# Kernel optimization log

Hardware: AMD Instinct MI355X
Metric: run time of the kernel (lower is better)

Reference implementation:

```python
import jax, jax.numpy as jnp
import numpy as np
from jax import lax

B, T = 2048, 256
V, E, H = 128, 128, 64
POS_WEIGHT = 20.0


def setup_inputs() -> dict:
    key = jax.random.key(0)
    ks = jax.random.split(key, 9)
    # indices in [1, V) so padding_idx=0 row (zeroed) is unused
    x = jax.random.randint(ks[0], (B, T), 1, V)
    targets = (jax.random.uniform(ks[1], (B,)) < 0.05).astype(jnp.float32)
    emb = jax.random.normal(ks[2], (V, E), dtype=jnp.float32).at[0].set(0.0)  # padding_idx=0
    k = 1.0 / np.sqrt(H)
    W_ih = jax.random.uniform(ks[3], (4 * H, E), minval=-k, maxval=k, dtype=jnp.float32)
    W_hh = jax.random.uniform(ks[4], (4 * H, H), minval=-k, maxval=k, dtype=jnp.float32)
    b_ih = jax.random.uniform(ks[5], (4 * H,), minval=-k, maxval=k, dtype=jnp.float32)
    b_hh = jax.random.uniform(ks[6], (4 * H,), minval=-k, maxval=k, dtype=jnp.float32)
    W_fc = jax.random.uniform(ks[7], (1, H), minval=-k, maxval=k, dtype=jnp.float32)
    b_fc = jax.random.uniform(ks[8], (1,), minval=-k, maxval=k, dtype=jnp.float32)
    return {"x": x, "targets": targets, "emb": emb, "W_ih": W_ih, "W_hh": W_hh,
            "b_ih": b_ih, "b_hh": b_hh, "W_fc": W_fc, "b_fc": b_fc}


def reference(x, targets, emb, W_ih, W_hh, b_ih, b_hh, W_fc, b_fc):
    xe = emb[x]  # [B, T, E]
    # precompute input-to-hidden projections for all timesteps: [B, T, 4H]
    xp = jnp.einsum('bte,ge->btg', xe, W_ih) + b_ih + b_hh
    h0 = jnp.zeros((xe.shape[0], W_hh.shape[1]), dtype=xe.dtype)
    c0 = jnp.zeros_like(h0)

    def step(carry, xt):
        h, c = carry
        gates = xt + h @ W_hh.T  # [B, 4H], PyTorch gate order: i, f, g, o
        i, f, g, o = jnp.split(gates, 4, axis=-1)
        c = jax.nn.sigmoid(f) * c + jax.nn.sigmoid(i) * jnp.tanh(g)
        h = jax.nn.sigmoid(o) * jnp.tanh(c)
        return (h, c), None

    (hT, _), _ = lax.scan(step, (h0, c0), jnp.swapaxes(xp, 0, 1))  # scan over time
    logits = (hT @ W_fc.T + b_fc)[:, 0]  # [B]
    # BCEWithLogits with pos_weight, mean reduction (numerically stable)
    loss = -(POS_WEIGHT * targets * jax.nn.log_sigmoid(logits)
             + (1.0 - targets) * jax.nn.log_sigmoid(-logits)).mean()
    return logits, loss
```

## Files before the change

### kernel.cpp

```cpp
#include <hip/hip_runtime.h>
#include <stdint.h>

#define B_ 2048
#define T_ 256
#define V_ 128
#define E_ 128
#define H_ 64
#define G4_ 256
#define POS_W 20.0f
#define MB_ 4
#define NBLK_ (B_ / MB_)
typedef _Float16 half1;
typedef __attribute__((ext_vector_type(8))) _Float16 f16x8;
typedef __attribute__((ext_vector_type(4))) float f32x4;

#if __has_builtin(__builtin_amdgcn_exp2f)
#define EXP2F(x) __builtin_amdgcn_exp2f(x)
#else
#define EXP2F(x) exp2f(x)
#endif

#if __has_builtin(__builtin_amdgcn_rcpf)
#define RCPF(x) __builtin_amdgcn_rcpf(x)
#else
#define RCPF(x) (1.0f / (x))
#endif

__device__ __forceinline__ float sigm(float x) {
    return RCPF(1.0f + EXP2F(-1.44269504f * x));
}
__device__ __forceinline__ float tanhr(float x) {
    float t = EXP2F(2.88539008f * x);
    return 1.0f - 2.0f * RCPF(t + 1.0f);
}

__device__ __forceinline__ void lds_barrier() {
    asm volatile("s_waitcnt lgkmcnt(0)\n\ts_barrier" ::: "memory");
}

__global__ void k_prep(const float* __restrict__ emb, const float* __restrict__ Wih,
                       const float* __restrict__ bih, const float* __restrict__ bhh,
                       float* __restrict__ projC, float* __restrict__ loss_slot) {
    int tid = threadIdx.x;
    int v = blockIdx.x;
    if (v == 0 && tid == 0) *loss_slot = 0.0f;
    int u = tid >> 2, g = tid & 3;
    int row = g * 64 + u;
    const float4* e4 = (const float4*)(emb + v * E_);
    const float4* w4 = (const float4*)(Wih + row * E_);
    float acc = bih[row] + bhh[row];
#pragma unroll
    for (int i = 0; i < E_ / 4; ++i) {
        float4 a = e4[i];
        float4 b = w4[i];
        acc += a.x * b.x + a.y * b.y + a.z * b.z + a.w * b.w;
    }
    projC[v * G4_ + tid] = acc;
}

__launch_bounds__(256, 2)
__global__ void k_lstm(const int* __restrict__ x, const float* __restrict__ Whh,
                       const float* __restrict__ projC, const float* __restrict__ Wfc,
                       const float* __restrict__ bfc, const float* __restrict__ targets,
                       float* __restrict__ logits, float* __restrict__ loss_slot) {
    int b0 = blockIdx.x * MB_;
    int t = threadIdx.x;
    int w = t >> 6, l = t & 63;
    int q = l >> 4, cc = l & 15;
    int u = 16 * w + cc;

    __shared__ __align__(16) half1 hf[2][1024];
    __shared__ int xT[T_][MB_];
    __shared__ float hfin[MB_][68];
    __shared__ float zred[MB_];

#pragma unroll
    for (int i = 0; i < MB_; ++i) xT[t][i] = x[(b0 + i) * T_ + t] << 10;
    ((float*)hf)[t] = 0.0f;
    ((float*)hf)[t + 256] = 0.0f;
    ((float*)hf)[t + 512] = 0.0f;
    ((float*)hf)[t + 768] = 0.0f;
    __syncthreads();

    f16x8 bf[4][2];
#pragma unroll
    for (int jj = 0; jj < 4; ++jj) {
#pragma unroll
        for (int c = 0; c < 2; ++c) {
            int row = jj * 64 + 16 * w + cc;
            int kb = c * 32 + q * 8;
            float4 w0 = *(const float4*)(Whh + row * H_ + kb);
            float4 w1 = *(const float4*)(Whh + row * H_ + kb + 4);
            f16x8 tmp;
            tmp[0] = (half1)w0.x; tmp[1] = (half1)w0.y;
            tmp[2] = (half1)w0.z; tmp[3] = (half1)w0.w;
            tmp[4] = (half1)w1.x; tmp[5] = (half1)w1.y;
            tmp[6] = (half1)w1.z; tmp[7] = (half1)w1.w;
            bf[jj][c] = tmp;
        }
    }

    int hbase = (u >> 5) * 512 + ((u >> 3) & 3) * 128 + (4 * q) * 8 + (u & 7);

    float cA = 0.0f, hA = 0.0f;
    const char* pcb = (const char*)projC;
    int uoff = u << 4;

    f32x4 ppA = *(const f32x4*)(pcb + xT[0][q] + uoff);
    f32x4 pnA = *(const f32x4*)(pcb + xT[1][q] + uoff);
    int xcA = xT[2][q];

    const f32x4 z4 = {0.0f, 0.0f, 0.0f, 0.0f};
    int p = 0;
#pragma unroll 2
    for (int step = 0; step < T_; ++step) {
        const f16x8 a0 = *(const f16x8*)(hf[p] + l * 8);
        const f16x8 a1 = *(const f16x8*)(hf[p] + 512 + l * 8);

        float gA[4];
#pragma unroll
        for (int jj = 0; jj < 4; ++jj) {
            f32x4 c4 = z4;
            c4[0] = ppA[jj];
            f32x4 d0 = __builtin_amdgcn_mfma_f32_16x16x32_f16(a0, bf[jj][0], c4, 0, 0, 0);
            f32x4 d1 = __builtin_amdgcn_mfma_f32_16x16x32_f16(a1, bf[jj][1], z4, 0, 0, 0);
            gA[jj] = d0[0] + d1[0];
        }

        f32x4 p2A = *(const f32x4*)(pcb + xcA + uoff);
        int xnA = xT[(step + 3) & (T_ - 1)][q];

        float iA = sigm(gA[0]);
        float fA = sigm(gA[1]);
        float ggA = tanhr(gA[2]);
        float oA = sigm(gA[3]);
        cA = fA * cA + iA * ggA;
        hA = oA * tanhr(cA);

        hf[p ^ 1][hbase] = (half1)hA;

        ppA = pnA;
        pnA = p2A;
        xcA = xnA;
        p ^= 1;
        lds_barrier();
    }

    hfin[q][u] = hA;
    __syncthreads();
    int m4 = t >> 6, uu = t & 63;
    float part = hfin[m4][uu] * Wfc[uu];
#pragma unroll
    for (int off = 32; off > 0; off >>= 1) part += __shfl_down(part, off, 64);
    if (uu == 0) {
        float z = part + bfc[0];
        logits[b0 + m4] = z;
        float tg = targets[b0 + m4];
        float e = EXP2F(-1.44269504f * fabsf(z));
        float lsp = fminf(z, 0.0f) - log1pf(e);
        float lsn = lsp - z;
        zred[m4] = -(POS_W * tg * lsp + (1.0f - tg) * lsn) * (1.0f / (float)B_);
    }
    __syncthreads();
    if (t == 0) {
        float s = 0.0f;
#pragma unroll
        for (int i = 0; i < MB_; ++i) s += zred[i];
        atomicAdd(loss_slot, s);
    }
}

extern "C" void kernel_launch(void* const* d_in, const int* in_sizes, int n_in,
                              void* d_out, int out_size, void* d_ws, size_t ws_size,
                              hipStream_t stream) {
    const int* x = (const int*)d_in[0];
    const float* targets = (const float*)d_in[1];
    const float* emb = (const float*)d_in[2];
    const float* Wih = (const float*)d_in[3];
    const float* Whh = (const float*)d_in[4];
    const float* bih = (const float*)d_in[5];
    const float* bhh = (const float*)d_in[6];
    const float* Wfc = (const float*)d_in[7];
    const float* bfc = (const float*)d_in[8];
    float* out = (float*)d_out;

    float* projC = (float*)d_ws;

    k_prep<<<dim3(V_), dim3(256), 0, stream>>>(emb, Wih, bih, bhh, projC, out + B_);
    k_lstm<<<dim3(NBLK_), dim3(256), 0, stream>>>(x, Whh, projC, Wfc, bfc, targets, out,
                                                  out + B_);
}
```

Baseline: 158.2 us.

## Ping-pong two batch groups per block to overlap MFMA with cell math

Each block now handles 8 sequences with 512 threads, split into two groups of 4 waves that run out of phase: while one group issues the recurrent MFMAs, the other computes gate nonlinearities and the cell update. Each group keeps its own h buffer, and the input projection is folded into the exponent argument instead of the MFMA accumulator. The goal is to hide MFMA latency behind transcendental ALU work inside the serial time loop. The cost is two barriers per step instead of one and half as many blocks, with occupancy now capped at one 512-thread block per CU by the launch bounds.

```diff
diff --git a/kernel.cpp b/kernel.cpp
--- a/kernel.cpp
+++ b/kernel.cpp
@@ -8,7 +8,7 @@
 #define H_ 64
 #define G4_ 256
 #define POS_W 20.0f
-#define MB_ 4
+#define MB_ 8
 #define NBLK_ (B_ / MB_)
 typedef _Float16 half1;
 typedef __attribute__((ext_vector_type(8))) _Float16 f16x8;
@@ -26,13 +26,7 @@
 #define RCPF(x) (1.0f / (x))
 #endif
 
-__device__ __forceinline__ float sigm(float x) {
-    return RCPF(1.0f + EXP2F(-1.44269504f * x));
-}
-__device__ __forceinline__ float tanhr(float x) {
-    float t = EXP2F(2.88539008f * x);
-    return 1.0f - 2.0f * RCPF(t + 1.0f);
-}
+#define L2E 1.44269504f
 
 __device__ __forceinline__ void lds_barrier() {
     asm volatile("s_waitcnt lgkmcnt(0)\n\ts_barrier" ::: "memory");
@@ -58,7 +52,7 @@
     projC[v * G4_ + tid] = acc;
 }
 
-__launch_bounds__(256, 2)
+__launch_bounds__(512, 1)
 __global__ void k_lstm(const int* __restrict__ x, const float* __restrict__ Whh,
                        const float* __restrict__ projC, const float* __restrict__ Wfc,
                        const float* __restrict__ bfc, const float* __restrict__ targets,
@@ -66,20 +60,22 @@
     int b0 = blockIdx.x * MB_;
     int t = threadIdx.x;
     int w = t >> 6, l = t & 63;
+    int g = w >> 2, wg = w & 3;
     int q = l >> 4, cc = l & 15;
-    int u = 16 * w + cc;
+    int u = 16 * wg + cc;
+    int r = g * 4 + q;
 
     __shared__ __align__(16) half1 hf[2][1024];
     __shared__ int xT[T_][MB_];
     __shared__ float hfin[MB_][68];
     __shared__ float zred[MB_];
 
-#pragma unroll
-    for (int i = 0; i < MB_; ++i) xT[t][i] = x[(b0 + i) * T_ + t] << 10;
+    for (int i = t; i < T_ * MB_; i += 512) {
+        int tt = i >> 3, rr = i & 7;
+        xT[tt][rr] = x[(b0 + rr) * T_ + tt] << 10;
+    }
     ((float*)hf)[t] = 0.0f;
-    ((float*)hf)[t + 256] = 0.0f;
     ((float*)hf)[t + 512] = 0.0f;
-    ((float*)hf)[t + 768] = 0.0f;
     __syncthreads();
 
     f16x8 bf[4][2];
@@ -87,7 +83,7 @@
     for (int jj = 0; jj < 4; ++jj) {
 #pragma unroll
         for (int c = 0; c < 2; ++c) {
-            int row = jj * 64 + 16 * w + cc;
+            int row = jj * 64 + 16 * wg + cc;
             int kb = c * 32 + q * 8;
             float4 w0 = *(const float4*)(Whh + row * H_ + kb);
             float4 w1 = *(const float4*)(Whh + row * H_ + kb + 4);
@@ -102,64 +98,84 @@
 
     int hbase = (u >> 5) * 512 + ((u >> 3) & 3) * 128 + (4 * q) * 8 + (u & 7);
 
-    float cA = 0.0f, hA = 0.0f;
+    float creg = 0.0f, hreg = 0.0f;
     const char* pcb = (const char*)projC;
     int uoff = u << 4;
 
-    f32x4 ppA = *(const f32x4*)(pcb + xT[0][q] + uoff);
-    f32x4 pnA = *(const f32x4*)(pcb + xT[1][q] + uoff);
-    int xcA = xT[2][q];
-
+    f32x4 pp = *(const f32x4*)(pcb + xT[0][r] + uoff);
+    f32x4 pn = *(const f32x4*)(pcb + xT[1][r] + uoff);
+    int xc = xT[2][r];
+
+    f32x4 d0[4], d1[4];
+    float psx = 0.f, psy = 0.f, pgz = 0.f, psw = 0.f;
     const f32x4 z4 = {0.0f, 0.0f, 0.0f, 0.0f};
-    int p = 0;
-#pragma unroll 2
+
+#define MFMA_HALF(STEP_)                                                              \
+    do {                                                                              \
+        const f16x8 a0 = *(const f16x8*)(hf[g] + l * 8);                              \
+        const f16x8 a1 = *(const f16x8*)(hf[g] + 512 + l * 8);                        \
+        _Pragma("unroll") for (int jj = 0; jj < 4; ++jj) {                            \
+            d0[jj] = __builtin_amdgcn_mfma_f32_16x16x32_f16(a0, bf[jj][0], z4, 0, 0, 0); \
+            d1[jj] = __builtin_amdgcn_mfma_f32_16x16x32_f16(a1, bf[jj][1], z4, 0, 0, 0); \
+        }                                                                             \
+        f32x4 p2 = *(const f32x4*)(pcb + xc + uoff);                                  \
+        int xn = xT[((STEP_) + 3) & (T_ - 1)][r];                                     \
+        psx = -L2E * pp.x;                                                            \
+        psy = -L2E * pp.y;                                                            \
+        pgz = 2.0f * L2E * pp.z;                                                      \
+        psw = -L2E * pp.w;                                                            \
+        pp = pn; pn = p2; xc = xn;                                                    \
+    } while (0)
+
+#define CELL_HALF()                                                                   \
+    do {                                                                              \
+        float g0v = d0[0][0] + d1[0][0];                                              \
+        float g1v = d0[1][0] + d1[1][0];                                              \
+        float g2v = d0[2][0] + d1[2][0];                                              \
+        float g3v = d0[3][0] + d1[3][0];                                              \
+        float ei = EXP2F(__builtin_fmaf(-L2E, g0v, psx));                             \
+        float ef = EXP2F(__builtin_fmaf(-L2E, g1v, psy));                             \
+        float eg = EXP2F(__builtin_fmaf(2.0f * L2E, g2v, pgz));                       \
+        float eo = EXP2F(__builtin_fmaf(-L2E, g3v, psw));                             \
+        float i_ = RCPF(1.0f + ei);                                                   \
+        float f_ = RCPF(1.0f + ef);                                                   \
+        float tg = 1.0f - 2.0f * RCPF(eg + 1.0f);                                     \
+        float o_ = RCPF(1.0f + eo);                                                   \
+        creg = __builtin_fmaf(f_, creg, i_ * tg);                                     \
+        float et = EXP2F(2.0f * L2E * creg);                                          \
+        hreg = o_ * (1.0f - 2.0f * RCPF(et + 1.0f));                                  \
+        hf[g][hbase] = (half1)hreg;                                                   \
+    } while (0)
+
     for (int step = 0; step < T_; ++step) {
-        const f16x8 a0 = *(const f16x8*)(hf[p] + l * 8);
-        const f16x8 a1 = *(const f16x8*)(hf[p] + 512 + l * 8);
-
-        float gA[4];
-#pragma unroll
-        for (int jj = 0; jj < 4; ++jj) {
-            f32x4 c4 = z4;
-            c4[0] = ppA[jj];
-            f32x4 d0 = __builtin_amdgcn_mfma_f32_16x16x32_f16(a0, bf[jj][0], c4, 0, 0, 0);
-            f32x4 d1 = __builtin_amdgcn_mfma_f32_16x16x32_f16(a1, bf[jj][1], z4, 0, 0, 0);
-            gA[jj] = d0[0] + d1[0];
+        if (g == 0) {
+            MFMA_HALF(step);
+        } else if (step) {
+            CELL_HALF();
         }
-
-        f32x4 p2A = *(const f32x4*)(pcb + xcA + uoff);
-        int xnA = xT[(step + 3) & (T_ - 1)][q];
-
-        float iA = sigm(gA[0]);
-        float fA = sigm(gA[1]);
-        float ggA = tanhr(gA[2]);
-        float oA = sigm(gA[3]);
-        cA = fA * cA + iA * ggA;
-        hA = oA * tanhr(cA);
-
-        hf[p ^ 1][hbase] = (half1)hA;
-
-        ppA = pnA;
-        pnA = p2A;
-        xcA = xnA;
-        p ^= 1;
         lds_barrier();
-    }
-
-    hfin[q][u] = hA;
+        if (g == 0) {
+            CELL_HALF();
+        } else {
+            MFMA_HALF(step);
+        }
+        lds_barrier();
+    }
+    if (g == 1) CELL_HALF();
+
+    hfin[r][u] = hreg;
     __syncthreads();
-    int m4 = t >> 6, uu = t & 63;
-    float part = hfin[m4][uu] * Wfc[uu];
+    float part = hfin[w][l] * Wfc[l];
 #pragma unroll
     for (int off = 32; off > 0; off >>= 1) part += __shfl_down(part, off, 64);
-    if (uu == 0) {
+    if (l == 0) {
         float z = part + bfc[0];
-        logits[b0 + m4] = z;
-        float tg = targets[b0 + m4];
-        float e = EXP2F(-1.44269504f * fabsf(z));
+        logits[b0 + w] = z;
+        float tg = targets[b0 + w];
+        float e = EXP2F(-L2E * fabsf(z));
         float lsp = fminf(z, 0.0f) - log1pf(e);
         float lsn = lsp - z;
-        zred[m4] = -(POS_W * tg * lsp + (1.0f - tg) * lsn) * (1.0f / (float)B_);
+        zred[w] = -(POS_W * tg * lsp + (1.0f - tg) * lsn) * (1.0f / (float)B_);
     }
     __syncthreads();
     if (t == 0) {
@@ -168,6 +184,8 @@
         for (int i = 0; i < MB_; ++i) s += zred[i];
         atomicAdd(loss_slot, s);
     }
+#undef MFMA_HALF
+#undef CELL_HALF
 }
 
 extern "C" void kernel_launch(void* const* d_in, const int* in_sizes, int n_in,
@@ -187,6 +205,6 @@
     float* projC = (float*)d_ws;
 
     k_prep<<<dim3(V_), dim3(256), 0, stream>>>(emb, Wih, bih, bhh, projC, out + B_);
-    k_lstm<<<dim3(NBLK_), dim3(256), 0, stream>>>(x, Whh, projC, Wfc, bfc, targets, out,
+    k_lstm<<<dim3(NBLK_), dim3(512), 0, stream>>>(x, Whh, projC, Wfc, bfc, targets, out,
                                                   out + B_);
 }
```

Result: slower. 186.9 us (+18.1%).
